# Kernel tuning notes

Measured on AMD Instinct MI355X. Metric: run time of the kernel, lower is better.

The kernel has to match this reference:

```python
import jax, jax.numpy as jnp
import numpy as np

B, S, D = 1, 1024, 2048          # batch, seq, hidden
H, KH, HD = 16, 16, 128          # heads, kv heads, head_dim
E, K, FI = 8, 4, 1408            # experts, top_k, moe_intermediate
FS = 5632                        # shared expert intermediate
WIN = 512                        # sliding window
THETA = 1.0e6                    # rope base
EPS = 1e-6                       # rmsnorm eps


def setup_inputs() -> dict:
    key = jax.random.key(0)
    ks = jax.random.split(key, 16)
    nrm = lambda k, shape: jax.random.normal(k, shape, jnp.float32) * 0.02
    return dict(
        hidden_states=jax.random.normal(ks[0], (B, S, D), jnp.float32),
        ln1_w=jnp.ones((D,), jnp.float32),
        ln2_w=jnp.ones((D,), jnp.float32),
        wq=nrm(ks[1], (D, H * HD)), bq=jnp.zeros((H * HD,), jnp.float32),
        wk=nrm(ks[2], (D, KH * HD)), bk=jnp.zeros((KH * HD,), jnp.float32),
        wv=nrm(ks[3], (D, KH * HD)), bv=jnp.zeros((KH * HD,), jnp.float32),
        wo=nrm(ks[4], (H * HD, D)),
        w_router=nrm(ks[5], (D, E)),
        w_gate_e=nrm(ks[6], (E, D, FI)),
        w_up_e=nrm(ks[7], (E, D, FI)),
        w_down_e=nrm(ks[8], (E, FI, D)),
        ws_gate=nrm(ks[9], (D, FS)),
        ws_up=nrm(ks[10], (D, FS)),
        ws_down=nrm(ks[11], (FS, D)),
        w_shared_gate=nrm(ks[12], (D, 1)),
    )


def _rms(h, w):
    v = jnp.mean(h * h, axis=-1, keepdims=True)
    return h * jax.lax.rsqrt(v + EPS) * w


def _rope(q, k):
    pos = jnp.arange(S, dtype=jnp.float32)
    inv = 1.0 / (THETA ** (jnp.arange(0, HD, 2, dtype=jnp.float32) / HD))
    ang = pos[:, None] * inv[None, :]                      # [S, HD/2]
    cos = jnp.concatenate([jnp.cos(ang)] * 2, -1)[None, :, None, :]
    sin = jnp.concatenate([jnp.sin(ang)] * 2, -1)[None, :, None, :]
    rot = lambda t: jnp.concatenate([-t[..., HD // 2:], t[..., :HD // 2]], -1)
    return q * cos + rot(q) * sin, k * cos + rot(k) * sin


def reference(hidden_states, ln1_w, ln2_w, wq, bq, wk, bk, wv, bv, wo,
              w_router, w_gate_e, w_up_e, w_down_e,
              ws_gate, ws_up, ws_down, w_shared_gate):
    x = hidden_states
    # --- sliding-window causal attention ---
    h = _rms(x, ln1_w)
    q = (h @ wq + bq).reshape(B, S, H, HD)
    k = (h @ wk + bk).reshape(B, S, KH, HD)
    v = (h @ wv + bv).reshape(B, S, KH, HD)
    q, k = _rope(q, k)
    scores = jnp.einsum('bqhd,bkhd->bhqk', q, k) * (HD ** -0.5)
    i = jnp.arange(S)[:, None]
    j = jnp.arange(S)[None, :]
    mask = (j <= i) & (i - j < WIN)                        # causal + window
    scores = jnp.where(mask[None, None], scores, jnp.finfo(scores.dtype).min)
    attn = jax.nn.softmax(scores, axis=-1)
    o = jnp.einsum('bhqk,bkhd->bqhd', attn, v).reshape(B, S, H * HD) @ wo
    x = x + o
    # --- sparse MoE block ---
    h = _rms(x, ln2_w)
    t = h.reshape(B * S, D)
    logits = (t @ w_router).astype(jnp.float32)
    probs = jax.nn.softmax(logits, axis=-1)                # [T, E]
    top_w, top_i = jax.lax.top_k(probs, K)                 # norm_topk_prob=False
    cw = jnp.zeros((B * S, E), probs.dtype).at[jnp.arange(B * S)[:, None], top_i].set(top_w)
    # routed experts (dense combine == gather/dispatch/grouped-GEMM/combine)
    g = jnp.einsum('td,edf->etf', t, w_gate_e)
    u = jnp.einsum('td,edf->etf', t, w_up_e)
    eo = jnp.einsum('etf,efd->etd', jax.nn.silu(g) * u, w_down_e)
    routed = jnp.einsum('te,etd->td', cw, eo)
    # shared expert with sigmoid gate
    shared = (jax.nn.silu(t @ ws_gate) * (t @ ws_up)) @ ws_down
    sgate = jax.nn.sigmoid(t @ w_shared_gate)              # [T, 1]
    moe = routed + sgate * shared
    return x + moe.reshape(B, S, D)
```

## Files before the change

### kernel.cpp

```cpp
#include <hip/hip_runtime.h>

#define S_ 1024
#define D_ 2048
#define H_ 16
#define HD_ 128
#define E_ 8
#define FI_ 1408
#define FS_ 5632
#define WIN_ 512
#define T_ 1024
#define QKVN 6144

typedef _Float16 f16;
typedef __attribute__((ext_vector_type(8))) _Float16 f16x8;
typedef __attribute__((ext_vector_type(4))) float f32x4;

#define MFMA16(a, b, c) __builtin_amdgcn_mfma_f32_16x16x32_f16((a), (b), (c), 0, 0, 0)

__device__ __forceinline__ void gload16(const void* g, void* l) {
    __builtin_amdgcn_global_load_lds(
        (const __attribute__((address_space(1))) unsigned*)g,
        (__attribute__((address_space(3))) unsigned*)l, 16, 0, 0);
}

__global__ __launch_bounds__(256) void rmsnorm16_kernel(const float* __restrict__ x,
                                                        const float* __restrict__ w,
                                                        f16* __restrict__ out) {
    int t = blockIdx.x;
    const float* xr = x + (long)t * D_;
    int base = threadIdx.x * 8;
    float4 v0 = *(const float4*)(xr + base);
    float4 v1 = *(const float4*)(xr + base + 4);
    float ss = v0.x*v0.x + v0.y*v0.y + v0.z*v0.z + v0.w*v0.w
             + v1.x*v1.x + v1.y*v1.y + v1.z*v1.z + v1.w*v1.w;
    #pragma unroll
    for (int off = 1; off < 64; off <<= 1) ss += __shfl_xor(ss, off);
    __shared__ float red[4];
    if ((threadIdx.x & 63) == 0) red[threadIdx.x >> 6] = ss;
    __syncthreads();
    float tot = red[0] + red[1] + red[2] + red[3];
    float scale = rsqrtf(tot / (float)D_ + 1e-6f);
    float4 w0 = *(const float4*)(w + base);
    float4 w1 = *(const float4*)(w + base + 4);
    f16x8 o;
    o[0] = (f16)(v0.x*scale*w0.x); o[1] = (f16)(v0.y*scale*w0.y);
    o[2] = (f16)(v0.z*scale*w0.z); o[3] = (f16)(v0.w*scale*w0.w);
    o[4] = (f16)(v1.x*scale*w1.x); o[5] = (f16)(v1.y*scale*w1.y);
    o[6] = (f16)(v1.z*scale*w1.z); o[7] = (f16)(v1.w*scale*w1.w);
    *(f16x8*)(out + (long)t * D_ + base) = o;
}

__global__ __launch_bounds__(256) void tconv_kernel(const float* __restrict__ src,
                                                    f16* __restrict__ dst,
                                                    int K, int N, long sSrc, long sDst,
                                                    int mode) {
    src += (long)blockIdx.z * sSrc;
    dst += (long)blockIdx.z * sDst;
    int n0 = blockIdx.x * 64, k0 = blockIdx.y * 64;
    __shared__ f16 tile[64][72];
    int t = threadIdx.x, r = t >> 2, c4 = (t & 3) * 16;
    const float* sp = src + (long)(k0 + r) * N + n0 + c4;
    #pragma unroll
    for (int i = 0; i < 16; i += 4) {
        float4 v = *(const float4*)(sp + i);
        tile[r][c4 + i + 0] = (f16)v.x; tile[r][c4 + i + 1] = (f16)v.y;
        tile[r][c4 + i + 2] = (f16)v.z; tile[r][c4 + i + 3] = (f16)v.w;
    }
    __syncthreads();
    int nr = n0 + r;
    long orow = (mode == 0) ? nr : ((long)(nr >> 4) * 32 + (nr & 15) + (mode == 2 ? 16 : 0));
    f16* dp = dst + orow * K + k0 + c4;
    #pragma unroll
    for (int i = 0; i < 16; i++) dp[i] = tile[c4 + i][r];
}

template <int EPI>
__global__ __launch_bounds__(256) void gemm16_kernel(
    const f16* __restrict__ Ag, const f16* __restrict__ BTg,
    void* Cg, const void* auxg, int M, int N, int K,
    long sA, long sB, long sC, long sAux) {
    int z = blockIdx.z;
    const f16* A = Ag + (long)z * sA;
    const f16* BT = BTg + (long)z * sB;
    int bm = blockIdx.y * 128, bn = blockIdx.x * 128;
    int tid = threadIdx.x, lane = tid & 63, wave = tid >> 6;
    int wm = (wave >> 1) * 64, wn = (wave & 1) * 64;

    __shared__ f16 As[128][64];
    __shared__ f16 Bs[128][64];

    f32x4 acc[4][4];
    #pragma unroll
    for (int i = 0; i < 4; i++)
        #pragma unroll
        for (int j = 0; j < 4; j++) acc[i][j] = (f32x4){0.f, 0.f, 0.f, 0.f};

    int srow = wave * 32 + (lane >> 3);
    int scol = (((lane & 7) ^ (lane >> 3)) * 8);
    const f16* Ab = A + (long)(bm + srow) * K + scol;
    const f16* Bb = BT + (long)(bn + srow) * K + scol;

    for (int k0 = 0; k0 < K; k0 += 64) {
        __syncthreads();
        #pragma unroll
        for (int i = 0; i < 4; i++) {
            gload16(Ab + (long)i * 8 * K + k0, &As[wave * 32 + i * 8][0]);
            gload16(Bb + (long)i * 8 * K + k0, &Bs[wave * 32 + i * 8][0]);
        }
        __syncthreads();
        #pragma unroll
        for (int kk = 0; kk < 64; kk += 32) {
            f16x8 af[4], bf[4];
            #pragma unroll
            for (int mi = 0; mi < 4; mi++) {
                int r = wm + mi * 16 + (lane & 15);
                int c = ((kk >> 3) + (lane >> 4)) ^ (r & 7);
                af[mi] = *(const f16x8*)((const char*)&As[r][0] + (c << 4));
            }
            #pragma unroll
            for (int ni = 0; ni < 4; ni++) {
                int r = wn + ni * 16 + (lane & 15);
                int c = ((kk >> 3) + (lane >> 4)) ^ (r & 7);
                bf[ni] = *(const f16x8*)((const char*)&Bs[r][0] + (c << 4));
            }
            #pragma unroll
            for (int mi = 0; mi < 4; mi++)
                #pragma unroll
                for (int ni = 0; ni < 4; ni++)
                    acc[mi][ni] = MFMA16(af[mi], bf[ni], acc[mi][ni]);
        }
    }

    if (EPI == 5) {
        int half = N >> 1;
        #pragma unroll
        for (int mi = 0; mi < 4; mi++) {
            #pragma unroll
            for (int p = 0; p < 2; p++) {
                #pragma unroll
                for (int i = 0; i < 4; i++) {
                    int m = bm + wm + mi * 16 + (lane >> 4) * 4 + i;
                    int j = ((bn + wn) >> 1) + p * 16 + (lane & 15);
                    float g = acc[mi][2 * p][i];
                    float u = acc[mi][2 * p + 1][i];
                    ((f16*)Cg + (long)z * sC)[(long)m * half + j] =
                        (f16)(g / (1.f + __expf(-g)) * u);
                }
            }
        }
        return;
    }
    #pragma unroll
    for (int mi = 0; mi < 4; mi++) {
        #pragma unroll
        for (int ni = 0; ni < 4; ni++) {
            #pragma unroll
            for (int i = 0; i < 4; i++) {
                int m = bm + wm + mi * 16 + (lane >> 4) * 4 + i;
                int n = bn + wn + ni * 16 + (lane & 15);
                long idx = (long)m * N + n;
                float v = acc[mi][ni][i];
                if (EPI == 0) {
                    ((f16*)Cg + (long)z * sC)[idx] = (f16)v;
                } else if (EPI == 1) {
                    ((f16*)Cg)[idx] = (f16)(v + ((const float*)auxg)[n]);
                } else if (EPI == 2) {
                    ((float*)Cg)[idx] = v + ((const float*)auxg)[idx];
                } else if (EPI == 4) {
                    ((float*)Cg)[idx] = v;
                }
            }
        }
    }
}

__global__ __launch_bounds__(256) void rope16_kernel(f16* __restrict__ qkv) {
    int s = blockIdx.x;
    float fs = (float)s;
    for (int p = threadIdx.x; p < H_ * 64; p += 256) {
        int h = p >> 6, j = p & 63;
        float inv = __expf(-(float)j * (13.815510557964274f / 64.f));
        float ang = fs * inv;
        float c = cosf(ang), sn = sinf(ang);
        long base = (long)s * QKVN + h * HD_ + j;
        float q1 = (float)qkv[base], q2 = (float)qkv[base + 64];
        qkv[base] = (f16)(q1 * c - q2 * sn);
        qkv[base + 64] = (f16)(q2 * c + q1 * sn);
        long kb = base + 2048;
        float k1 = (float)qkv[kb], k2 = (float)qkv[kb + 64];
        qkv[kb] = (f16)(k1 * c - k2 * sn);
        qkv[kb + 64] = (f16)(k2 * c + k1 * sn);
    }
}

__global__ __launch_bounds__(256) void attn16_kernel(const f16* __restrict__ qkv,
                                                     f16* __restrict__ Og) {
    int qt = blockIdx.x * 64;
    int head = blockIdx.y;
    int tid = threadIdx.x, lane = tid & 63, wave = tid >> 6;

    __shared__ f16 Ks[64][128];
    __shared__ f16 Vrow[64][128];
    __shared__ f16 VsT[128][64];
    __shared__ f16 Ps[4][16][64];

    int qr = qt + wave * 16 + (lane & 15);
    const f16* Qp = qkv + (long)qr * QKVN + head * HD_;
    f16x8 qf[4];
    #pragma unroll
    for (int kk = 0; kk < 4; kk++)
        qf[kk] = *(const f16x8*)(Qp + kk * 32 + (lane >> 4) * 8);

    f32x4 oacc[8];
    #pragma unroll
    for (int db = 0; db < 8; db++) oacc[db] = (f32x4){0.f, 0.f, 0.f, 0.f};
    float m_run[4] = {-1e30f, -1e30f, -1e30f, -1e30f};
    float l_run[4] = {0.f, 0.f, 0.f, 0.f};

    int k_lo = qt - (WIN_ - 1);
    if (k_lo < 0) k_lo = 0;
    k_lo &= ~63;

    for (int k0 = k_lo; k0 < qt + 64; k0 += 64) {
        __syncthreads();
        {
            int row = tid >> 2, cq = (tid & 3) * 32;
            const f16* Kp = qkv + (long)(k0 + row) * QKVN + 2048 + head * HD_ + cq;
            const f16* Vp = Kp + 2048;
            #pragma unroll
            for (int u = 0; u < 32; u += 8) {
                f16x8 tk = *(const f16x8*)(Kp + u);
                int co = ((cq + u) * 2) ^ ((row & 7) << 4);
                *(f16x8*)((char*)&Ks[row][0] + co) = tk;
                *(f16x8*)(&Vrow[row][cq + u]) = *(const f16x8*)(Vp + u);
            }
        }
        __syncthreads();
        {
            int d = tid >> 1, ks = (tid & 1) * 32;
            f16 tmp[32];
            #pragma unroll
            for (int j = 0; j < 32; j++) tmp[j] = Vrow[ks + j][d];
            #pragma unroll
            for (int u = 0; u < 32; u += 8) {
                int co = ((ks + u) * 2) ^ ((d & 7) << 4);
                f16x8 tv;
                #pragma unroll
                for (int j = 0; j < 8; j++) tv[j] = tmp[u + j];
                *(f16x8*)((char*)&VsT[d][0] + co) = tv;
            }
        }
        f32x4 sacc[4];
        #pragma unroll
        for (int cb = 0; cb < 4; cb++) sacc[cb] = (f32x4){0.f, 0.f, 0.f, 0.f};
        #pragma unroll
        for (int kk = 0; kk < 4; kk++) {
            #pragma unroll
            for (int cb = 0; cb < 4; cb++) {
                int krow = cb * 16 + (lane & 15);
                int co = ((kk * 32 + (lane >> 4) * 8) * 2) ^ ((krow & 7) << 4);
                f16x8 kf = *(const f16x8*)((const char*)&Ks[krow][0] + co);
                sacc[cb] = MFMA16(qf[kk], kf, sacc[cb]);
            }
        }
        float mtile[4] = {-1e30f, -1e30f, -1e30f, -1e30f};
        #pragma unroll
        for (int cb = 0; cb < 4; cb++) {
            #pragma unroll
            for (int i = 0; i < 4; i++) {
                int qi = qt + wave * 16 + (lane >> 4) * 4 + i;
                int kj = k0 + cb * 16 + (lane & 15);
                float s = sacc[cb][i] * 0.08838834764831845f;
                bool valid = (kj <= qi) && (qi - kj < WIN_);
                s = valid ? s : -1e30f;
                sacc[cb][i] = s;
                mtile[i] = fmaxf(mtile[i], s);
            }
        }
        #pragma unroll
        for (int i = 0; i < 4; i++) {
            float v = mtile[i];
            v = fmaxf(v, __shfl_xor(v, 1));
            v = fmaxf(v, __shfl_xor(v, 2));
            v = fmaxf(v, __shfl_xor(v, 4));
            v = fmaxf(v, __shfl_xor(v, 8));
            mtile[i] = v;
        }
        float pscale[4], lsum[4];
        #pragma unroll
        for (int i = 0; i < 4; i++) {
            float mnew = fmaxf(m_run[i], mtile[i]);
            pscale[i] = __expf(m_run[i] - mnew);
            m_run[i] = mnew;
            lsum[i] = 0.f;
        }
        #pragma unroll
        for (int cb = 0; cb < 4; cb++) {
            #pragma unroll
            for (int i = 0; i < 4; i++) {
                float mn = fmaxf(m_run[i], -1e20f);
                float p = __expf(sacc[cb][i] - mn);
                lsum[i] += p;
                int prow = (lane >> 4) * 4 + i;
                int pcol = cb * 16 + (lane & 15);
                int co = (pcol * 2) ^ ((prow & 7) << 4);
                *(f16*)((char*)&Ps[wave][prow][0] + co) = (f16)p;
            }
        }
        #pragma unroll
        for (int i = 0; i < 4; i++) {
            float v = lsum[i];
            v += __shfl_xor(v, 1);
            v += __shfl_xor(v, 2);
            v += __shfl_xor(v, 4);
            v += __shfl_xor(v, 8);
            l_run[i] = l_run[i] * pscale[i] + v;
        }
        #pragma unroll
        for (int db = 0; db < 8; db++)
            #pragma unroll
            for (int i = 0; i < 4; i++) oacc[db][i] *= pscale[i];
        __syncthreads();
        #pragma unroll
        for (int ks = 0; ks < 2; ks++) {
            int prow = lane & 15;
            int co = ((ks * 32 + (lane >> 4) * 8) * 2) ^ ((prow & 7) << 4);
            f16x8 pf = *(const f16x8*)((const char*)&Ps[wave][prow][0] + co);
            #pragma unroll
            for (int db = 0; db < 8; db++) {
                int vrow2 = db * 16 + (lane & 15);
                int co2 = ((ks * 32 + (lane >> 4) * 8) * 2) ^ ((vrow2 & 7) << 4);
                f16x8 vf = *(const f16x8*)((const char*)&VsT[vrow2][0] + co2);
                oacc[db] = MFMA16(pf, vf, oacc[db]);
            }
        }
    }
    #pragma unroll
    for (int db = 0; db < 8; db++) {
        #pragma unroll
        for (int i = 0; i < 4; i++) {
            int qi = qt + wave * 16 + (lane >> 4) * 4 + i;
            int d = db * 16 + (lane & 15);
            Og[(long)qi * D_ + head * HD_ + d] = (f16)(oacc[db][i] / l_run[i]);
        }
    }
}

__global__ __launch_bounds__(256) void router_kernel(
    const float* __restrict__ x2, const float* __restrict__ ln2,
    const float* __restrict__ wr, const float* __restrict__ wshg,
    float* __restrict__ cw, float* __restrict__ sgate) {
    int t = blockIdx.x;
    const float* xr = x2 + (long)t * D_;
    int base = threadIdx.x * 8;
    float xv[8];
    *(float4*)&xv[0] = *(const float4*)(xr + base);
    *(float4*)&xv[4] = *(const float4*)(xr + base + 4);
    float ss = 0.f;
    #pragma unroll
    for (int j = 0; j < 8; j++) ss += xv[j] * xv[j];
    #pragma unroll
    for (int off = 1; off < 64; off <<= 1) ss += __shfl_xor(ss, off);
    __shared__ float red0[4];
    if ((threadIdx.x & 63) == 0) red0[threadIdx.x >> 6] = ss;
    __syncthreads();
    float scale = rsqrtf((red0[0] + red0[1] + red0[2] + red0[3]) / (float)D_ + 1e-6f);

    float part[9] = {0.f,0.f,0.f,0.f,0.f,0.f,0.f,0.f,0.f};
    #pragma unroll
    for (int j = 0; j < 8; j++) {
        int d = base + j;
        float hv = xv[j] * scale * ln2[d];
        const float* wrow = wr + (long)d * E_;
        #pragma unroll
        for (int e = 0; e < 8; e++) part[e] += hv * wrow[e];
        part[8] += hv * wshg[d];
    }
    #pragma unroll
    for (int e = 0; e < 9; e++) {
        float v = part[e];
        #pragma unroll
        for (int off = 1; off < 64; off <<= 1) v += __shfl_xor(v, off);
        part[e] = v;
    }
    __shared__ float red[4][9];
    int lane = threadIdx.x & 63, wave = threadIdx.x >> 6;
    if (lane == 0)
        #pragma unroll
        for (int e = 0; e < 9; e++) red[wave][e] = part[e];
    __syncthreads();
    if (threadIdx.x == 0) {
        float logit[9];
        #pragma unroll
        for (int e = 0; e < 9; e++) logit[e] = red[0][e] + red[1][e] + red[2][e] + red[3][e];
        float mx = logit[0];
        #pragma unroll
        for (int e = 1; e < 8; e++) mx = fmaxf(mx, logit[e]);
        float p[8], sum = 0.f;
        #pragma unroll
        for (int e = 0; e < 8; e++) { p[e] = expf(logit[e] - mx); sum += p[e]; }
        #pragma unroll
        for (int e = 0; e < 8; e++) p[e] /= sum;
        float sel[8] = {0.f,0.f,0.f,0.f,0.f,0.f,0.f,0.f};
        float tmp[8];
        #pragma unroll
        for (int e = 0; e < 8; e++) tmp[e] = p[e];
        for (int it = 0; it < 4; it++) {
            int best = 0;
            float bvv = tmp[0];
            #pragma unroll
            for (int e = 1; e < 8; e++)
                if (tmp[e] > bvv) { bvv = tmp[e]; best = e; }
            sel[best] = p[best];
            tmp[best] = -1.f;
        }
        #pragma unroll
        for (int e = 0; e < 8; e++) cw[(long)e * T_ + t] = sel[e];
        sgate[t] = 1.f / (1.f + expf(-logit[8]));
    }
}

__global__ __launch_bounds__(256) void biascat_kernel(const float* bq, const float* bk,
                                                      const float* bv, float* bqkv) {
    int i = blockIdx.x * 256 + threadIdx.x;
    if (i < 2048) bqkv[i] = bq[i];
    else if (i < 4096) bqkv[i] = bk[i - 2048];
    else if (i < 6144) bqkv[i] = bv[i - 4096];
}

__global__ __launch_bounds__(256) void acc4_kernel(const f16* __restrict__ eo4,
                                                   const float* __restrict__ cwb,
                                                   float* __restrict__ routed, int first) {
    long nv = (long)T_ * D_ / 8;
    for (long i = (long)blockIdx.x * blockDim.x + threadIdx.x; i < nv;
         i += (long)gridDim.x * blockDim.x) {
        int t = (int)(i >> 8);
        float w0 = cwb[t], w1 = cwb[T_ + t], w2 = cwb[2 * T_ + t], w3 = cwb[3 * T_ + t];
        const long es = (long)T_ * D_;
        f16x8 e0 = *(const f16x8*)(eo4 + i * 8);
        f16x8 e1 = *(const f16x8*)(eo4 + es + i * 8);
        f16x8 e2 = *(const f16x8*)(eo4 + 2 * es + i * 8);
        f16x8 e3 = *(const f16x8*)(eo4 + 3 * es + i * 8);
        float r[8];
        #pragma unroll
        for (int j = 0; j < 8; j++)
            r[j] = w0 * (float)e0[j] + w1 * (float)e1[j] + w2 * (float)e2[j] + w3 * (float)e3[j];
        float* rp = routed + i * 8;
        if (first) {
            #pragma unroll
            for (int j = 0; j < 8; j++) rp[j] = r[j];
        } else {
            #pragma unroll
            for (int j = 0; j < 8; j++) rp[j] += r[j];
        }
    }
}

__global__ __launch_bounds__(256) void combine_kernel(
    const float* __restrict__ x2, const float* __restrict__ routed,
    const float* __restrict__ sho, const float* __restrict__ sg,
    float* __restrict__ out) {
    long total = (long)T_ * D_ / 4;
    for (long i = (long)blockIdx.x * blockDim.x + threadIdx.x; i < total;
         i += (long)gridDim.x * blockDim.x) {
        int t = (int)(i >> 9);
        float4 a = ((const float4*)x2)[i];
        float4 r = ((const float4*)routed)[i];
        float4 s = ((const float4*)sho)[i];
        float g = sg[t];
        float4 o;
        o.x = a.x + r.x + g * s.x;
        o.y = a.y + r.y + g * s.y;
        o.z = a.z + r.z + g * s.z;
        o.w = a.w + r.w + g * s.w;
        ((float4*)out)[i] = o;
    }
}

extern "C" void kernel_launch(void* const* d_in, const int* in_sizes, int n_in,
                              void* d_out, int out_size, void* d_ws, size_t ws_size,
                              hipStream_t stream) {
    const float* x    = (const float*)d_in[0];
    const float* ln1  = (const float*)d_in[1];
    const float* ln2  = (const float*)d_in[2];
    const float* wq   = (const float*)d_in[3];
    const float* bq   = (const float*)d_in[4];
    const float* wk   = (const float*)d_in[5];
    const float* bk   = (const float*)d_in[6];
    const float* wv   = (const float*)d_in[7];
    const float* bv   = (const float*)d_in[8];
    const float* wo   = (const float*)d_in[9];
    const float* wrt  = (const float*)d_in[10];
    const float* wge  = (const float*)d_in[11];
    const float* wue  = (const float*)d_in[12];
    const float* wde  = (const float*)d_in[13];
    const float* wsg  = (const float*)d_in[14];
    const float* wsu  = (const float*)d_in[15];
    const float* wsd  = (const float*)d_in[16];
    const float* wshg = (const float*)d_in[17];

    float* ws = (float*)d_ws;
    f16*   wT     = (f16*)ws;
    float* x2     = ws + 11534336;
    float* sho    = x2 + 2097152;
    float* bqkv   = sho + 2097152;
    float* cw     = bqkv + 6144;
    float* sg     = cw + 8192;
    f16*   h1     = (f16*)(sg + 1024);
    f16*   h2     = (f16*)(sg + 1024 + 1048576);
    float* poolG  = sg + 1024 + 2097152;
    float* slotI  = poolG + 5767168;
    float* routed = slotI + 4194304;
    f16*   qkv    = (f16*)poolG;
    f16*   Gg     = (f16*)poolG;
    f16*   sgb    = (f16*)slotI;
    f16*   eo4    = (f16*)slotI;
    f16*   ao     = h1;

    dim3 blk(256);

    rmsnorm16_kernel<<<T_, blk, 0, stream>>>(x, ln1, h1);
    biascat_kernel<<<24, blk, 0, stream>>>(bq, bk, bv, bqkv);
    tconv_kernel<<<dim3(32, 32, 1), blk, 0, stream>>>(wq, wT, 2048, 2048, 0, 0, 0);
    tconv_kernel<<<dim3(32, 32, 1), blk, 0, stream>>>(wk, wT + 2048L * 2048, 2048, 2048, 0, 0, 0);
    tconv_kernel<<<dim3(32, 32, 1), blk, 0, stream>>>(wv, wT + 4096L * 2048, 2048, 2048, 0, 0, 0);
    gemm16_kernel<1><<<dim3(48, 8, 1), blk, 0, stream>>>(h1, wT, qkv, bqkv,
                                                         T_, QKVN, D_, 0, 0, 0, 0);
    rope16_kernel<<<S_, blk, 0, stream>>>(qkv);
    attn16_kernel<<<dim3(16, 16), blk, 0, stream>>>(qkv, ao);
    tconv_kernel<<<dim3(32, 32, 1), blk, 0, stream>>>(wo, wT, 2048, 2048, 0, 0, 0);
    gemm16_kernel<2><<<dim3(16, 8, 1), blk, 0, stream>>>(ao, wT, x2, x,
                                                         T_, D_, D_, 0, 0, 0, 0);

    rmsnorm16_kernel<<<T_, blk, 0, stream>>>(x2, ln2, h2);
    router_kernel<<<T_, blk, 0, stream>>>(x2, ln2, wrt, wshg, cw, sg);

    tconv_kernel<<<dim3(88, 32, 1), blk, 0, stream>>>(wsg, wT, 2048, 5632, 0, 0, 1);
    tconv_kernel<<<dim3(88, 32, 1), blk, 0, stream>>>(wsu, wT, 2048, 5632, 0, 0, 2);
    gemm16_kernel<5><<<dim3(88, 8, 1), blk, 0, stream>>>(h2, wT, sgb, nullptr,
                                                         T_, 2 * FS_, D_, 0, 0, 0, 0);
    tconv_kernel<<<dim3(32, 88, 1), blk, 0, stream>>>(wsd, wT, 5632, 2048, 0, 0, 0);
    gemm16_kernel<4><<<dim3(16, 8, 1), blk, 0, stream>>>(sgb, wT, sho, nullptr,
                                                         T_, D_, FS_, 0, 0, 0, 0);

    tconv_kernel<<<dim3(22, 32, 4), blk, 0, stream>>>(wge, wT, 2048, 1408,
                                                      2048L * 1408, 2816L * 2048, 1);
    tconv_kernel<<<dim3(22, 32, 4), blk, 0, stream>>>(wue, wT, 2048, 1408,
                                                      2048L * 1408, 2816L * 2048, 2);
    gemm16_kernel<5><<<dim3(22, 8, 4), blk, 0, stream>>>(h2, wT, Gg, nullptr,
        T_, 2 * FI_, D_, 0, 2816L * 2048, 1024L * 1408, 0);
    tconv_kernel<<<dim3(22, 32, 4), blk, 0, stream>>>(wge + 4L * 2048 * 1408, wT, 2048, 1408,
                                                      2048L * 1408, 2816L * 2048, 1);
    tconv_kernel<<<dim3(22, 32, 4), blk, 0, stream>>>(wue + 4L * 2048 * 1408, wT, 2048, 1408,
                                                      2048L * 1408, 2816L * 2048, 2);
    gemm16_kernel<5><<<dim3(22, 8, 4), blk, 0, stream>>>(h2, wT, Gg + 4L * 1024 * 1408, nullptr,
        T_, 2 * FI_, D_, 0, 2816L * 2048, 1024L * 1408, 0);

    tconv_kernel<<<dim3(32, 22, 4), blk, 0, stream>>>(wde, wT, 1408, 2048,
                                                      1408L * 2048, 2048L * 1408, 0);
    gemm16_kernel<0><<<dim3(16, 8, 4), blk, 0, stream>>>(Gg, wT, eo4, nullptr,
        T_, D_, FI_, 1024L * 1408, 2048L * 1408, 1024L * 2048, 0);
    acc4_kernel<<<1024, blk, 0, stream>>>(eo4, cw, routed, 1);
    tconv_kernel<<<dim3(32, 22, 4), blk, 0, stream>>>(wde + 4L * 1408 * 2048, wT, 1408, 2048,
                                                      1408L * 2048, 2048L * 1408, 0);
    gemm16_kernel<0><<<dim3(16, 8, 4), blk, 0, stream>>>(Gg + 4L * 1024 * 1408, wT, eo4, nullptr,
        T_, D_, FI_, 1024L * 1408, 2048L * 1408, 1024L * 2048, 0);
    acc4_kernel<<<1024, blk, 0, stream>>>(eo4, cw + 4 * T_, routed, 0);

    combine_kernel<<<1024, blk, 0, stream>>>(x2, routed, sho, sg, (float*)d_out);
}
```

Before: 682.0 us.

## Route tokens to experts sparsely and split-K the wo and shared-down GEMMs

Adds a bucket kernel that compacts each expert's selected tokens into index and weight lists. The expert gate/up GEMM now gathers only routed rows and skips empty row tiles, and the down GEMM scales its output by the routing weight. The combine kernel gathers each token's expert outputs through a position map, which replaces the dense acc4 accumulation. The wo projection and shared-down GEMM are split along K into partial buffers that separate reduce kernels sum, giving more blocks in flight at the cost of extra fp32 traffic and two more launches.

```diff
diff --git a/kernel.cpp b/kernel.cpp
--- a/kernel.cpp
+++ b/kernel.cpp
@@ -13,6 +13,7 @@
 
 typedef _Float16 f16;
 typedef __attribute__((ext_vector_type(8))) _Float16 f16x8;
+typedef __attribute__((ext_vector_type(4))) _Float16 f16x4;
 typedef __attribute__((ext_vector_type(4))) float f32x4;
 
 #define MFMA16(a, b, c) __builtin_amdgcn_mfma_f32_16x16x32_f16((a), (b), (c), 0, 0, 0)
@@ -74,15 +75,23 @@
     for (int i = 0; i < 16; i++) dp[i] = tile[c4 + i][r];
 }
 
-template <int EPI>
+template <int EPI, int MODE>
 __global__ __launch_bounds__(256) void gemm16_kernel(
     const f16* __restrict__ Ag, const f16* __restrict__ BTg,
-    void* Cg, const void* auxg, int M, int N, int K,
-    long sA, long sB, long sC, long sAux) {
+    void* Cg, const void* auxg,
+    const int* __restrict__ tokidx, const int* __restrict__ cntv,
+    const float* __restrict__ tw,
+    int M, int N, int K, int lda, int ldb,
+    long sA, long sB, long sC) {
     int z = blockIdx.z;
     const f16* A = Ag + (long)z * sA;
     const f16* BT = BTg + (long)z * sB;
     int bm = blockIdx.y * 128, bn = blockIdx.x * 128;
+    int cnt = M;
+    if (MODE >= 1) {
+        cnt = cntv[z];
+        if (bm >= cnt) return;
+    }
     int tid = threadIdx.x, lane = tid & 63, wave = tid >> 6;
     int wm = (wave >> 1) * 64, wn = (wave & 1) * 64;
 
@@ -95,17 +104,30 @@
         #pragma unroll
         for (int j = 0; j < 4; j++) acc[i][j] = (f32x4){0.f, 0.f, 0.f, 0.f};
 
-    int srow = wave * 32 + (lane >> 3);
-    int scol = (((lane & 7) ^ (lane >> 3)) * 8);
-    const f16* Ab = A + (long)(bm + srow) * K + scol;
-    const f16* Bb = BT + (long)(bn + srow) * K + scol;
+    int srow8 = lane >> 3;
+    int scol = ((lane & 7) ^ srow8) * 8;
+    const f16* Abp[4];
+    const f16* Bbp[4];
+    #pragma unroll
+    for (int i = 0; i < 4; i++) {
+        int ra = bm + wave * 32 + i * 8 + srow8;
+        long arow;
+        if (MODE == 1) {
+            int tok = (ra < cnt) ? tokidx[z * T_ + ra] : 0;
+            arow = tok;
+        } else {
+            arow = ra;
+        }
+        Abp[i] = A + arow * (long)lda + scol;
+        Bbp[i] = BT + (long)(bn + wave * 32 + i * 8 + srow8) * ldb + scol;
+    }
 
     for (int k0 = 0; k0 < K; k0 += 64) {
         __syncthreads();
         #pragma unroll
         for (int i = 0; i < 4; i++) {
-            gload16(Ab + (long)i * 8 * K + k0, &As[wave * 32 + i * 8][0]);
-            gload16(Bb + (long)i * 8 * K + k0, &Bs[wave * 32 + i * 8][0]);
+            gload16(Abp[i] + k0, &As[wave * 32 + i * 8][0]);
+            gload16(Bbp[i] + k0, &Bs[wave * 32 + i * 8][0]);
         }
         __syncthreads();
         #pragma unroll
@@ -160,14 +182,13 @@
                 int n = bn + wn + ni * 16 + (lane & 15);
                 long idx = (long)m * N + n;
                 float v = acc[mi][ni][i];
-                if (EPI == 0) {
-                    ((f16*)Cg + (long)z * sC)[idx] = (f16)v;
-                } else if (EPI == 1) {
+                if (EPI == 1) {
                     ((f16*)Cg)[idx] = (f16)(v + ((const float*)auxg)[n]);
-                } else if (EPI == 2) {
-                    ((float*)Cg)[idx] = v + ((const float*)auxg)[idx];
                 } else if (EPI == 4) {
-                    ((float*)Cg)[idx] = v;
+                    ((float*)Cg + (long)z * sC)[idx] = v;
+                } else if (EPI == 6) {
+                    float wv = tw[z * T_ + m];
+                    ((f16*)Cg + (long)z * sC)[idx] = (f16)(v * wv);
                 }
             }
         }
@@ -420,6 +441,29 @@
     }
 }
 
+__global__ __launch_bounds__(512) void bucket_kernel(const float* __restrict__ cw,
+                                                     int* __restrict__ cnt,
+                                                     int* __restrict__ tokidx,
+                                                     float* __restrict__ tw,
+                                                     int* __restrict__ posmat) {
+    int e = threadIdx.x >> 6, lane = threadIdx.x & 63;
+    int count = 0;
+    for (int base = 0; base < T_; base += 64) {
+        int t = base + lane;
+        float wv = cw[(long)e * T_ + t];
+        unsigned long long m = __ballot(wv > 0.f);
+        int pre = __popcll(m & ((1ull << lane) - 1ull));
+        if (wv > 0.f) {
+            int s = count + pre;
+            tokidx[e * T_ + s] = t;
+            tw[e * T_ + s] = wv;
+            posmat[e * T_ + t] = s;
+        }
+        count += __popcll(m);
+    }
+    if (lane == 0) cnt[e] = count;
+}
+
 __global__ __launch_bounds__(256) void biascat_kernel(const float* bq, const float* bk,
                                                       const float* bv, float* bqkv) {
     int i = blockIdx.x * 256 + threadIdx.x;
@@ -428,51 +472,64 @@
     else if (i < 6144) bqkv[i] = bv[i - 4096];
 }
 
-__global__ __launch_bounds__(256) void acc4_kernel(const f16* __restrict__ eo4,
-                                                   const float* __restrict__ cwb,
-                                                   float* __restrict__ routed, int first) {
-    long nv = (long)T_ * D_ / 8;
-    for (long i = (long)blockIdx.x * blockDim.x + threadIdx.x; i < nv;
-         i += (long)gridDim.x * blockDim.x) {
-        int t = (int)(i >> 8);
-        float w0 = cwb[t], w1 = cwb[T_ + t], w2 = cwb[2 * T_ + t], w3 = cwb[3 * T_ + t];
-        const long es = (long)T_ * D_;
-        f16x8 e0 = *(const f16x8*)(eo4 + i * 8);
-        f16x8 e1 = *(const f16x8*)(eo4 + es + i * 8);
-        f16x8 e2 = *(const f16x8*)(eo4 + 2 * es + i * 8);
-        f16x8 e3 = *(const f16x8*)(eo4 + 3 * es + i * 8);
-        float r[8];
-        #pragma unroll
-        for (int j = 0; j < 8; j++)
-            r[j] = w0 * (float)e0[j] + w1 * (float)e1[j] + w2 * (float)e2[j] + w3 * (float)e3[j];
-        float* rp = routed + i * 8;
-        if (first) {
-            #pragma unroll
-            for (int j = 0; j < 8; j++) rp[j] = r[j];
-        } else {
-            #pragma unroll
-            for (int j = 0; j < 8; j++) rp[j] += r[j];
-        }
+__global__ __launch_bounds__(256) void reduce2r_kernel(const float* __restrict__ x,
+                                                       const float* __restrict__ p,
+                                                       float* __restrict__ out) {
+    long total = (long)T_ * D_ / 4;
+    for (long i = (long)blockIdx.x * 256 + threadIdx.x; i < total;
+         i += (long)gridDim.x * 256) {
+        float4 a = ((const float4*)x)[i];
+        float4 b = ((const float4*)p)[i];
+        float4 c = ((const float4*)p)[i + total];
+        float4 o;
+        o.x = a.x + b.x + c.x; o.y = a.y + b.y + c.y;
+        o.z = a.z + b.z + c.z; o.w = a.w + b.w + c.w;
+        ((float4*)out)[i] = o;
+    }
+}
+
+__global__ __launch_bounds__(256) void reduce4_kernel(const float* __restrict__ p,
+                                                      float* __restrict__ out) {
+    long total = (long)T_ * D_ / 4;
+    for (long i = (long)blockIdx.x * 256 + threadIdx.x; i < total;
+         i += (long)gridDim.x * 256) {
+        float4 a = ((const float4*)p)[i];
+        float4 b = ((const float4*)p)[i + total];
+        float4 c = ((const float4*)p)[i + 2 * total];
+        float4 d = ((const float4*)p)[i + 3 * total];
+        float4 o;
+        o.x = a.x + b.x + c.x + d.x; o.y = a.y + b.y + c.y + d.y;
+        o.z = a.z + b.z + c.z + d.z; o.w = a.w + b.w + c.w + d.w;
+        ((float4*)out)[i] = o;
     }
 }
 
 __global__ __launch_bounds__(256) void combine_kernel(
-    const float* __restrict__ x2, const float* __restrict__ routed,
-    const float* __restrict__ sho, const float* __restrict__ sg,
+    const float* __restrict__ x2, const float* __restrict__ sho,
+    const float* __restrict__ sg, const float* __restrict__ cw,
+    const int* __restrict__ posmat, const f16* __restrict__ eo,
     float* __restrict__ out) {
     long total = (long)T_ * D_ / 4;
-    for (long i = (long)blockIdx.x * blockDim.x + threadIdx.x; i < total;
-         i += (long)gridDim.x * blockDim.x) {
+    for (long i = (long)blockIdx.x * 256 + threadIdx.x; i < total;
+         i += (long)gridDim.x * 256) {
         int t = (int)(i >> 9);
+        int c4 = (int)(i & 511) * 4;
         float4 a = ((const float4*)x2)[i];
-        float4 r = ((const float4*)routed)[i];
         float4 s = ((const float4*)sho)[i];
         float g = sg[t];
-        float4 o;
-        o.x = a.x + r.x + g * s.x;
-        o.y = a.y + r.y + g * s.y;
-        o.z = a.z + r.z + g * s.z;
-        o.w = a.w + r.w + g * s.w;
+        float r0 = a.x + g * s.x, r1 = a.y + g * s.y;
+        float r2 = a.z + g * s.z, r3 = a.w + g * s.w;
+        #pragma unroll
+        for (int e = 0; e < 8; e++) {
+            float w = cw[(long)e * T_ + t];
+            if (w > 0.f) {
+                int slot = posmat[(long)e * T_ + t];
+                f16x4 v = *(const f16x4*)(eo + ((long)e * T_ + slot) * D_ + c4);
+                r0 += (float)v[0]; r1 += (float)v[1];
+                r2 += (float)v[2]; r3 += (float)v[3];
+            }
+        }
+        float4 o; o.x = r0; o.y = r1; o.z = r2; o.w = r3;
         ((float4*)out)[i] = o;
     }
 }
@@ -506,16 +563,21 @@
     float* bqkv   = sho + 2097152;
     float* cw     = bqkv + 6144;
     float* sg     = cw + 8192;
-    f16*   h1     = (f16*)(sg + 1024);
-    f16*   h2     = (f16*)(sg + 1024 + 1048576);
-    float* poolG  = sg + 1024 + 2097152;
-    float* slotI  = poolG + 5767168;
-    float* routed = slotI + 4194304;
-    f16*   qkv    = (f16*)poolG;
-    f16*   Gg     = (f16*)poolG;
-    f16*   sgb    = (f16*)slotI;
-    f16*   eo4    = (f16*)slotI;
-    f16*   ao     = h1;
+    int*   cnt    = (int*)(sg + 1024);
+    int*   tokidx = cnt + 8;
+    float* tw     = (float*)(tokidx + 8192);
+    int*   posmat = (int*)(tw + 8192);
+    f16*   h1     = (f16*)(posmat + 8192);
+    f16*   h2     = (f16*)((float*)h1 + 1048576);
+    float* pool   = (float*)h2 + 1048576;
+
+    f16*   qkv     = (f16*)pool;
+    float* woparts = pool + 3145728;
+    f16*   sgb     = (f16*)pool;
+    float* parts4  = pool + 2883584;
+    f16*   Gg      = (f16*)pool;
+    f16*   eo      = (f16*)(pool + 5767168);
+    f16*   ao      = h1;
 
     dim3 blk(256);
 
@@ -524,48 +586,57 @@
     tconv_kernel<<<dim3(32, 32, 1), blk, 0, stream>>>(wq, wT, 2048, 2048, 0, 0, 0);
     tconv_kernel<<<dim3(32, 32, 1), blk, 0, stream>>>(wk, wT + 2048L * 2048, 2048, 2048, 0, 0, 0);
     tconv_kernel<<<dim3(32, 32, 1), blk, 0, stream>>>(wv, wT + 4096L * 2048, 2048, 2048, 0, 0, 0);
-    gemm16_kernel<1><<<dim3(48, 8, 1), blk, 0, stream>>>(h1, wT, qkv, bqkv,
-                                                         T_, QKVN, D_, 0, 0, 0, 0);
+    gemm16_kernel<1, 0><<<dim3(48, 8, 1), blk, 0, stream>>>(
+        h1, wT, qkv, bqkv, nullptr, nullptr, nullptr,
+        T_, QKVN, D_, 2048, 2048, 0, 0, 0);
     rope16_kernel<<<S_, blk, 0, stream>>>(qkv);
     attn16_kernel<<<dim3(16, 16), blk, 0, stream>>>(qkv, ao);
     tconv_kernel<<<dim3(32, 32, 1), blk, 0, stream>>>(wo, wT, 2048, 2048, 0, 0, 0);
-    gemm16_kernel<2><<<dim3(16, 8, 1), blk, 0, stream>>>(ao, wT, x2, x,
-                                                         T_, D_, D_, 0, 0, 0, 0);
+    gemm16_kernel<4, 0><<<dim3(16, 8, 2), blk, 0, stream>>>(
+        ao, wT, woparts, nullptr, nullptr, nullptr, nullptr,
+        T_, D_, 1024, 2048, 2048, 1024, 1024, 2097152);
+    reduce2r_kernel<<<512, blk, 0, stream>>>(x, woparts, x2);
 
     rmsnorm16_kernel<<<T_, blk, 0, stream>>>(x2, ln2, h2);
     router_kernel<<<T_, blk, 0, stream>>>(x2, ln2, wrt, wshg, cw, sg);
+    bucket_kernel<<<1, 512, 0, stream>>>(cw, cnt, tokidx, tw, posmat);
 
     tconv_kernel<<<dim3(88, 32, 1), blk, 0, stream>>>(wsg, wT, 2048, 5632, 0, 0, 1);
     tconv_kernel<<<dim3(88, 32, 1), blk, 0, stream>>>(wsu, wT, 2048, 5632, 0, 0, 2);
-    gemm16_kernel<5><<<dim3(88, 8, 1), blk, 0, stream>>>(h2, wT, sgb, nullptr,
-                                                         T_, 2 * FS_, D_, 0, 0, 0, 0);
+    gemm16_kernel<5, 0><<<dim3(88, 8, 1), blk, 0, stream>>>(
+        h2, wT, sgb, nullptr, nullptr, nullptr, nullptr,
+        T_, 2 * FS_, D_, 2048, 2048, 0, 0, 0);
     tconv_kernel<<<dim3(32, 88, 1), blk, 0, stream>>>(wsd, wT, 5632, 2048, 0, 0, 0);
-    gemm16_kernel<4><<<dim3(16, 8, 1), blk, 0, stream>>>(sgb, wT, sho, nullptr,
-                                                         T_, D_, FS_, 0, 0, 0, 0);
+    gemm16_kernel<4, 0><<<dim3(16, 8, 4), blk, 0, stream>>>(
+        sgb, wT, parts4, nullptr, nullptr, nullptr, nullptr,
+        T_, D_, 1408, 5632, 5632, 1408, 1408, 2097152);
+    reduce4_kernel<<<512, blk, 0, stream>>>(parts4, sho);
 
     tconv_kernel<<<dim3(22, 32, 4), blk, 0, stream>>>(wge, wT, 2048, 1408,
                                                       2048L * 1408, 2816L * 2048, 1);
     tconv_kernel<<<dim3(22, 32, 4), blk, 0, stream>>>(wue, wT, 2048, 1408,
                                                       2048L * 1408, 2816L * 2048, 2);
-    gemm16_kernel<5><<<dim3(22, 8, 4), blk, 0, stream>>>(h2, wT, Gg, nullptr,
-        T_, 2 * FI_, D_, 0, 2816L * 2048, 1024L * 1408, 0);
+    gemm16_kernel<5, 1><<<dim3(22, 8, 4), blk, 0, stream>>>(
+        h2, wT, Gg, nullptr, tokidx, cnt, nullptr,
+        T_, 2 * FI_, D_, 2048, 2048, 0, 2816L * 2048, 1024L * 1408);
     tconv_kernel<<<dim3(22, 32, 4), blk, 0, stream>>>(wge + 4L * 2048 * 1408, wT, 2048, 1408,
                                                       2048L * 1408, 2816L * 2048, 1);
     tconv_kernel<<<dim3(22, 32, 4), blk, 0, stream>>>(wue + 4L * 2048 * 1408, wT, 2048, 1408,
                                                       2048L * 1408, 2816L * 2048, 2);
-    gemm16_kernel<5><<<dim3(22, 8, 4), blk, 0, stream>>>(h2, wT, Gg + 4L * 1024 * 1408, nullptr,
-        T_, 2 * FI_, D_, 0, 2816L * 2048, 1024L * 1408, 0);
+    gemm16_kernel<5, 1><<<dim3(22, 8, 4), blk, 0, stream>>>(
+        h2, wT, Gg + 4L * 1024 * 1408, nullptr, tokidx + 4 * T_, cnt + 4, nullptr,
+        T_, 2 * FI_, D_, 2048, 2048, 0, 2816L * 2048, 1024L * 1408);
 
     tconv_kernel<<<dim3(32, 22, 4), blk, 0, stream>>>(wde, wT, 1408, 2048,
                                                       1408L * 2048, 2048L * 1408, 0);
-    gemm16_kernel<0><<<dim3(16, 8, 4), blk, 0, stream>>>(Gg, wT, eo4, nullptr,
-        T_, D_, FI_, 1024L * 1408, 2048L * 1408, 1024L * 2048, 0);
-    acc4_kernel<<<1024, blk, 0, stream>>>(eo4, cw, routed, 1);
+    gemm16_kernel<6, 2><<<dim3(16, 8, 4), blk, 0, stream>>>(
+        Gg, wT, eo, nullptr, nullptr, cnt, tw,
+        T_, D_, 1408, 1408, 1408, 1024L * 1408, 2048L * 1408, 1024L * 2048);
     tconv_kernel<<<dim3(32, 22, 4), blk, 0, stream>>>(wde + 4L * 1408 * 2048, wT, 1408, 2048,
                                                       1408L * 2048, 2048L * 1408, 0);
-    gemm16_kernel<0><<<dim3(16, 8, 4), blk, 0, stream>>>(Gg + 4L * 1024 * 1408, wT, eo4, nullptr,
-        T_, D_, FI_, 1024L * 1408, 2048L * 1408, 1024L * 2048, 0);
-    acc4_kernel<<<1024, blk, 0, stream>>>(eo4, cw + 4 * T_, routed, 0);
-
-    combine_kernel<<<1024, blk, 0, stream>>>(x2, routed, sho, sg, (float*)d_out);
-}
+    gemm16_kernel<6, 2><<<dim3(16, 8, 4), blk, 0, stream>>>(
+        Gg + 4L * 1024 * 1408, wT, eo + 4L * 1024 * 2048, nullptr, nullptr, cnt + 4, tw + 4 * T_,
+        T_, D_, 1408, 1408, 1408, 1024L * 1408, 2048L * 1408, 1024L * 2048);
+
+    combine_kernel<<<1024, blk, 0, stream>>>(x2, sho, sg, cw, posmat, eo, (float*)d_out);
+}
```

New measurement: 603.3 us. 1.13x faster.
